# Performance work log

Hardware: AMD Instinct MI355X
Metric: run time of the kernel (lower is better)

Reference implementation:

```python
import jax, jax.numpy as jnp
import numpy as np

B, S, H, ZD, IN = 256, 64, 128, 128, 2


def _gru_cell(x, h, W_ih, W_hh, b_ih, b_hh):
    # PyTorch GRU cell math
    gi = x @ W_ih.T + b_ih
    gh = h @ W_hh.T + b_hh
    i_r, i_z, i_n = jnp.split(gi, 3, axis=-1)
    h_r, h_z, h_n = jnp.split(gh, 3, axis=-1)
    r = jax.nn.sigmoid(i_r + h_r)
    z = jax.nn.sigmoid(i_z + h_z)
    n = jnp.tanh(i_n + r * h_n)
    return (1.0 - z) * n + z * h


def setup_inputs() -> dict:
    key = jax.random.key(0)
    ks = jax.random.split(key, 20)
    instance = jax.random.uniform(ks[0], (B, S, IN), dtype=jnp.float32)
    # solution must be a valid tour (permutation per batch row)
    solution = jax.vmap(lambda k: jax.random.permutation(k, S))(
        jax.random.split(ks[1], B)).astype(jnp.int32)
    Z = jax.random.normal(ks[2], (B, ZD), dtype=jnp.float32)
    instance_hidden = jax.random.normal(ks[3], (B, S, H), dtype=jnp.float32)
    last_hh = jnp.zeros((B, H), jnp.float32)
    s = 0.1
    params = dict(
        W_emb=jax.random.normal(ks[4], (IN, H), jnp.float32) * s,
        b_emb=jnp.zeros((H,), jnp.float32),
        W_ih=jax.random.normal(ks[5], (3 * H, H), jnp.float32) * s,
        W_hh=jax.random.normal(ks[6], (3 * H, H), jnp.float32) * s,
        b_ih=jnp.zeros((3 * H,), jnp.float32),
        b_hh=jnp.zeros((3 * H,), jnp.float32),
        W_a=jax.random.normal(ks[7], (2 * H, H), jnp.float32) * s,
        v_a=jax.random.normal(ks[8], (H,), jnp.float32) * s,
        W1=jax.random.normal(ks[9], (2 * H + ZD, 2 * H), jnp.float32) * s,
        b1=jnp.zeros((2 * H,), jnp.float32),
        W2=jax.random.normal(ks[10], (2 * H, H), jnp.float32) * s,
        b2=jnp.zeros((H,), jnp.float32),
        Wp=jax.random.normal(ks[11], (2 * H, H), jnp.float32) * s,
        vp=jax.random.normal(ks[12], (H,), jnp.float32) * s,
    )
    return dict(instance=instance, solution=solution, Z=Z,
                instance_hidden=instance_hidden, last_hh=last_hh, **params)


def reference(instance, solution, Z, instance_hidden, last_hh,
              W_emb, b_emb, W_ih, W_hh, b_ih, b_hh,
              W_a, v_a, W1, b1, W2, b2, Wp, vp):
    b, s, _ = instance.shape
    barange = jnp.arange(b)
    mask0 = jnp.ones((b, s), instance.dtype).at[barange, solution[:, 0]].set(0.0)
    ref0 = instance[barange, solution[:, 0]]  # [B, IN]

    def step(carry, ptr_j):
        h, mask, ref_in = carry
        ref_h = ref_in @ W_emb + b_emb                       # [B,H] reference embedding
        h = _gru_cell(ref_h, h, W_ih, W_hh, b_ih, b_hh)      # [B,H] rnn step
        # encoder attention over static instance_hidden
        ha = jnp.concatenate([instance_hidden,
                              jnp.broadcast_to(h[:, None, :], instance_hidden.shape)], axis=2)
        attn = jax.nn.softmax(jnp.tanh(ha @ W_a) @ v_a, axis=1)      # [B,S]
        context = jnp.einsum('bs,bsh->bh', attn, instance_hidden)    # [B,H]
        fc_in = jnp.concatenate([context, Z, ref_h], axis=1)         # [B,2H+ZD]
        fco = (fc_in @ W1 + b1) @ W2 + b2                            # [B,H] fc1 -> fc2 (no activation)
        hp = jnp.concatenate([instance_hidden,
                              jnp.broadcast_to(fco[:, None, :], instance_hidden.shape)], axis=2)
        logits = jnp.tanh(hp @ Wp) @ vp                              # [B,S] pointer scores
        logprobs = jax.nn.log_softmax(logits + jnp.log(mask), axis=1)
        logp = logprobs[barange, ptr_j]                              # teacher-forced log-prob
        pred = jnp.argmax(logprobs, axis=1)
        mask = mask.at[barange, ptr_j].set(0.0)
        ref_in = instance[barange, ptr_j]
        return (h, mask, ref_in), (pred, logp)

    ptrs = solution[:, 1:].T                                         # [S-1, B]
    _, (preds, logps) = jax.lax.scan(step, (last_hh, mask0, ref0), ptrs)
    tour_idx = jnp.concatenate([solution[:, :1], preds.T.astype(solution.dtype)], axis=1)
    tour_logp = logps.T                                              # [B, S-1]
    return tour_idx, tour_logp
```

## Files before the change

### kernel.cpp

```cpp
#include <hip/hip_runtime.h>
#include <math.h>

#define NB 256
#define NS 64
#define NH 128
#define NZ 128
#define NSTEPS 63
#define HP 144
#define PP 132
#define SP 68

#define OFF_PREA 0
#define OFF_PREP 8448
#define OFF_WN   0
#define OFF_HALL 16896
#define OFF_ATTH 26112
#define OFF_SCOR 34560
#define OFF_U    38912
#define OFF_VA   39296
#define OFF_VPV  39424
#define OFF_REFX 39552
#define OFF_REFY 39616
#define OFF_SOL  39680
#define OFF_RANK 39744
#define OFF_SVA  39808
#define OFF_SVP  39809
#define SM_FLOATS 39812
#define OFF_GPRE 34560
#define OFF_BHH  35712

#define WS_WF   0
#define WS_WZ   16384
#define WS_U    32768
#define WS_GPRE 33152
#define WS_FLOATS 34304

__device__ __forceinline__ int padh(int i) { return i + ((i >> 5) << 2); }

__device__ __forceinline__ float ftanh(float x) {
  float e = __expf(2.0f * x);
  return 1.0f - 2.0f * __builtin_amdgcn_rcpf(e + 1.0f);
}
__device__ __forceinline__ float fsigm(float x) {
  return __builtin_amdgcn_rcpf(1.0f + __expf(-x));
}

#define PIN8(a, i)                                                          \
  asm volatile("" : "+v"((a)[(i)]), "+v"((a)[(i) + 1]), "+v"((a)[(i) + 2]), \
                    "+v"((a)[(i) + 3]), "+v"((a)[(i) + 4]),                 \
                    "+v"((a)[(i) + 5]), "+v"((a)[(i) + 6]),                 \
                    "+v"((a)[(i) + 7]))

__global__ __launch_bounds__(128, 1) void fold_kernel(
    const float* __restrict__ W1, const float* __restrict__ W2,
    const float* __restrict__ Wp, const float* __restrict__ W_ih,
    const float* __restrict__ W_emb, const float* __restrict__ b_emb,
    const float* __restrict__ b_ih, const float* __restrict__ b1,
    const float* __restrict__ b2, float* __restrict__ ws) {
  __shared__ float srow[NH];
  __shared__ float amS[256];
  const int g = blockIdx.x;
  const int o = threadIdx.x;
  if (g < 256) {
    const int r = (g < 128) ? g : (NH + (g - 128));
    const float* w1r = W1 + r * 256;
    float acc = 0.f;
#pragma unroll 16
    for (int m = 0; m < 256; ++m) acc += w1r[m] * W2[m * NH + o];
    srow[o] = acc;
    __syncthreads();
    float wf = 0.f;
#pragma unroll 16
    for (int j = 0; j < NH; ++j) wf += srow[j] * Wp[(NH + j) * NH + o];
    if (g < 128) ws[WS_WF + g * NH + o] = wf;
    else         ws[WS_WZ + (g - 128) * NH + o] = wf;
    if (g >= 1 && g <= 3) {
      const int row = (g - 1) * NH + o;
      const float* wi = W_ih + row * NH;
      float g0 = 0.f, g1 = 0.f, g2 = 0.f;
#pragma unroll 8
      for (int k4 = 0; k4 < 32; ++k4) {
        float4 w = *(const float4*)(wi + 4 * k4);
        float4 e0 = *(const float4*)(W_emb + 4 * k4);
        float4 e1 = *(const float4*)(W_emb + NH + 4 * k4);
        float4 eb = *(const float4*)(b_emb + 4 * k4);
        g0 += w.x * e0.x + w.y * e0.y + w.z * e0.z + w.w * e0.w;
        g1 += w.x * e1.x + w.y * e1.y + w.z * e1.z + w.w * e1.w;
        g2 += w.x * eb.x + w.y * eb.y + w.z * eb.z + w.w * eb.w;
      }
      ws[WS_GPRE + row] = g0;
      ws[WS_GPRE + 384 + row] = g1;
      ws[WS_GPRE + 768 + row] = g2 + b_ih[row];
    }
  } else {
    const int c = g - 256;
    const float* ev = (c == 0) ? W_emb : (c == 1) ? (W_emb + NH) : b_emb;
#pragma unroll
    for (int half = 0; half < 2; ++half) {
      const int m = o + 128 * half;
      float a = 0.f;
#pragma unroll 8
      for (int k = 0; k < NH; ++k) a += ev[k] * W1[(2 * NH + k) * 256 + m];
      amS[m] = (c == 2) ? (a + b1[m]) : a;
    }
    __syncthreads();
    float vv = (c == 2) ? b2[o] : 0.f;
#pragma unroll 16
    for (int m = 0; m < 256; ++m) vv += amS[m] * W2[m * NH + o];
    srow[o] = vv;
    __syncthreads();
    float U = 0.f;
#pragma unroll 16
    for (int j = 0; j < NH; ++j) U += srow[j] * Wp[(NH + j) * NH + o];
    ws[WS_U + c * NH + o] = U;
  }
}

__global__ __launch_bounds__(1024, 1) void decoder_kernel(
    const float* __restrict__ instance, const int* __restrict__ solution,
    const float* __restrict__ Z, const float* __restrict__ IH,
    const float* __restrict__ last_hh, const float* __restrict__ W_hh,
    const float* __restrict__ b_hh, const float* __restrict__ W_a,
    const float* __restrict__ v_a, const float* __restrict__ Wp,
    const float* __restrict__ vp, const float* __restrict__ ws,
    float* __restrict__ out) {
  extern __shared__ float sm[];
  int* soli = (int*)(sm + OFF_SOL);
  int* ranki = (int*)(sm + OFF_RANK);
  const int b = blockIdx.x;
  const int t = threadIdx.x;
  const float* ihb = IH + b * NS * NH;

  const int oc = t >> 3, qc = t & 7;
  const int oq = (t & 31) * 4, jg = t >> 5;
  const int jj = t >> 4, sq = t & 15;

  if (t < NS) {
    int sv = solution[b * NS + t];
    soli[t] = sv;
    ranki[sv] = t;
    sm[OFF_REFX + t] = instance[(b * NS + sv) * 2 + 0];
    sm[OFF_REFY + t] = instance[(b * NS + sv) * 2 + 1];
  }
  if (t < NH) {
    sm[OFF_VA + t] = v_a[t];
    sm[OFF_VPV + t] = vp[t];
    sm[OFF_HALL + padh(t)] = last_hh[b * NH + t];
  }
  if (t < 128) {
    const float* vsrc = (t < 64) ? v_a : vp;
    int u = t & 63;
    float s2 = vsrc[u] + vsrc[u + 64];
#pragma unroll
    for (int off = 32; off > 0; off >>= 1) s2 += __shfl_xor(s2, off);
    if (u == 0) sm[(t < 64) ? OFF_SVA : OFF_SVP] = s2;
  }
  if (t < 384) sm[OFF_BHH + t] = b_hh[t];
  for (int i = t; i < 1152; i += 1024) sm[OFF_GPRE + i] = ws[WS_GPRE + i];
  if (t < 256) sm[OFF_U + t] = ws[WS_U + t];
  {
    const float* zb = Z + b * NZ;
    float acc = 0.f;
#pragma unroll 4
    for (int u = 0; u < 16; ++u) {
      int k = 16 * qc + u;
      acc += zb[k] * ws[WS_WZ + k * NH + oc];
    }
    acc += __shfl_xor(acc, 1); acc += __shfl_xor(acc, 2); acc += __shfl_xor(acc, 4);
    if (qc == 0) sm[OFF_U + 2 * NH + oc] = ws[WS_U + 2 * NH + oc] + acc;
  }
  if (t < 512) {
    const int o4 = t >> 2, q4 = t & 3;
    const float* wnp = W_hh + (2 * NH + o4) * NH + 32 * q4;
#pragma unroll
    for (int u4 = 0; u4 < 8; ++u4) {
      float4 w = *(const float4*)(wnp + 4 * u4);
      sm[OFF_WN + t * 33 + 4 * u4 + 0] = w.x;
      sm[OFF_WN + t * 33 + 4 * u4 + 1] = w.y;
      sm[OFF_WN + t * 33 + 4 * u4 + 2] = w.z;
      sm[OFF_WN + t * 33 + 4 * u4 + 3] = w.w;
    }
  }
  if (t == 0) out[b * NS] = (float)soli[0];
  __syncthreads();

  {
    float whr[16], whz[16];
    {
      const float* br = W_hh + oc * NH + 16 * qc;
      const float* bz = W_hh + (NH + oc) * NH + 16 * qc;
#pragma unroll
      for (int u4 = 0; u4 < 4; ++u4) {
        float4 r4 = *(const float4*)(br + 4 * u4);
        float4 z4 = *(const float4*)(bz + 4 * u4);
        whr[4 * u4 + 0] = r4.x; whr[4 * u4 + 1] = r4.y;
        whr[4 * u4 + 2] = r4.z; whr[4 * u4 + 3] = r4.w;
        whz[4 * u4 + 0] = z4.x; whz[4 * u4 + 1] = z4.y;
        whz[4 * u4 + 2] = z4.z; whz[4 * u4 + 3] = z4.w;
      }
    }
    PIN8(whr, 0); PIN8(whr, 8);
    PIN8(whz, 0); PIN8(whz, 8);
    const float* wn = sm + OFF_WN + (oc * 4 + (qc >> 1)) * 33 + (qc & 1) * 16;
    const int hoffc = padh(16 * qc);
    const float bhr = sm[OFF_BHH + oc];
    const float bhz = sm[OFF_BHH + NH + oc];
    const float bhn = sm[OFF_BHH + 2 * NH + oc];
    const float gr0 = sm[OFF_GPRE + oc];
    const float gr1 = sm[OFF_GPRE + 384 + oc];
    const float gr2 = sm[OFF_GPRE + 768 + oc];
    const float gz0 = sm[OFF_GPRE + NH + oc];
    const float gz1 = sm[OFF_GPRE + 384 + NH + oc];
    const float gz2 = sm[OFF_GPRE + 768 + NH + oc];
    const float gn0 = sm[OFF_GPRE + 2 * NH + oc];
    const float gn1 = sm[OFF_GPRE + 384 + 2 * NH + oc];
    const float gn2 = sm[OFF_GPRE + 768 + 2 * NH + oc];
#pragma unroll 1
    for (int j = 1; j <= NSTEPS; ++j) {
      float ar = 0.f, az = 0.f, an = 0.f;
      const float* hp = sm + OFF_HALL + (j - 1) * HP + hoffc;
#pragma unroll
      for (int u = 0; u < 4; ++u) {
        float4 hv = *(const float4*)(hp + 4 * u);
        ar += hv.x * whr[4 * u] + hv.y * whr[4 * u + 1] +
              hv.z * whr[4 * u + 2] + hv.w * whr[4 * u + 3];
        az += hv.x * whz[4 * u] + hv.y * whz[4 * u + 1] +
              hv.z * whz[4 * u + 2] + hv.w * whz[4 * u + 3];
        an += hv.x * wn[4 * u] + hv.y * wn[4 * u + 1] +
              hv.z * wn[4 * u + 2] + hv.w * wn[4 * u + 3];
      }
      ar += __shfl_xor(ar, 1); ar += __shfl_xor(ar, 2); ar += __shfl_xor(ar, 4);
      az += __shfl_xor(az, 1); az += __shfl_xor(az, 2); az += __shfl_xor(az, 4);
      an += __shfl_xor(an, 1); an += __shfl_xor(an, 2); an += __shfl_xor(an, 4);
      if (qc == 0) {
        float r0 = sm[OFF_REFX + (j - 1)], r1 = sm[OFF_REFY + (j - 1)];
        float gir = r0 * gr0 + r1 * gr1 + gr2;
        float giz = r0 * gz0 + r1 * gz1 + gz2;
        float gin = r0 * gn0 + r1 * gn1 + gn2;
        float r = fsigm(gir + ar + bhr);
        float z = fsigm(giz + az + bhz);
        float n = ftanh(gin + r * (an + bhn));
        float hold = sm[OFF_HALL + (j - 1) * HP + padh(oc)];
        sm[OFF_HALL + j * HP + padh(oc)] = (1.f - z) * n + z * hold;
      }
      __syncthreads();
    }
  }

  for (int i = 4 * t; i < NS * NH; i += 4096)
    *(float4*)(sm + OFF_ATTH + i) = *(const float4*)(ihb + i);
  __syncthreads();
  {
    const int jx = t & 127, sg = t >> 7;
    float accA[8], accP[8];
#pragma unroll
    for (int si = 0; si < 8; ++si) { accA[si] = 0.f; accP[si] = 0.f; }
#pragma unroll 2
    for (int k4 = 0; k4 < 32; ++k4) {
      const int k = 4 * k4;
      float wa0 = W_a[(k + 0) * NH + jx];
      float wa1 = W_a[(k + 1) * NH + jx];
      float wa2 = W_a[(k + 2) * NH + jx];
      float wa3 = W_a[(k + 3) * NH + jx];
      float wp0 = Wp[(k + 0) * NH + jx];
      float wp1 = Wp[(k + 1) * NH + jx];
      float wp2 = Wp[(k + 2) * NH + jx];
      float wp3 = Wp[(k + 3) * NH + jx];
#pragma unroll
      for (int si = 0; si < 8; ++si) {
        float4 ih = *(const float4*)(sm + OFF_ATTH + (sg * 8 + si) * NH + k);
        accA[si] += ih.x * wa0 + ih.y * wa1 + ih.z * wa2 + ih.w * wa3;
        accP[si] += ih.x * wp0 + ih.y * wp1 + ih.z * wp2 + ih.w * wp3;
      }
    }
#pragma unroll
    for (int si = 0; si < 8; ++si) {
      sm[OFF_PREA + (sg * 8 + si) * PP + jx] = __expf(2.f * accA[si]);
      sm[OFF_PREP + (sg * 8 + si) * PP + jx] = __expf(2.f * accP[si]);
    }
  }
  __syncthreads();

  {
    float4 acc[2];
    acc[0] = (float4){0.f, 0.f, 0.f, 0.f};
    acc[1] = (float4){0.f, 0.f, 0.f, 0.f};
    const float* wbase = W_a + NH * NH + oq;
#pragma unroll 4
    for (int k4 = 0; k4 < 32; ++k4) {
      int k = 4 * k4;
      int hoff = k + 4 * (k4 >> 3);
      float4 w0 = *(const float4*)(wbase + (k + 0) * NH);
      float4 w1 = *(const float4*)(wbase + (k + 1) * NH);
      float4 w2 = *(const float4*)(wbase + (k + 2) * NH);
      float4 w3 = *(const float4*)(wbase + (k + 3) * NH);
#pragma unroll
      for (int i = 0; i < 2; ++i) {
        float4 hv = *(const float4*)(sm + OFF_HALL + (jg + 32 * i) * HP + hoff);
        acc[i].x += hv.x * w0.x + hv.y * w1.x + hv.z * w2.x + hv.w * w3.x;
        acc[i].y += hv.x * w0.y + hv.y * w1.y + hv.z * w2.y + hv.w * w3.y;
        acc[i].z += hv.x * w0.z + hv.y * w1.z + hv.z * w2.z + hv.w * w3.z;
        acc[i].w += hv.x * w0.w + hv.y * w1.w + hv.z * w2.w + hv.w * w3.w;
      }
    }
#pragma unroll
    for (int i = 0; i < 2; ++i) {
      float4 tv;
      tv.x = __expf(2.f * acc[i].x); tv.y = __expf(2.f * acc[i].y);
      tv.z = __expf(2.f * acc[i].z); tv.w = __expf(2.f * acc[i].w);
      *(float4*)(sm + OFF_ATTH + (jg + 32 * i) * PP + oq) = tv;
    }
  }
  __syncthreads();

  {
    const float sva = sm[OFF_SVA];
    const float* ah = sm + OFF_ATTH + jj * PP;
    float accv[4] = {0.f, 0.f, 0.f, 0.f};
#pragma unroll 2
    for (int k4 = 0; k4 < 32; ++k4) {
      float4 h = *(const float4*)(ah + 4 * k4);
      float4 v = *(const float4*)(sm + OFF_VA + 4 * k4);
#pragma unroll
      for (int i = 0; i < 4; ++i) {
        float4 a = *(const float4*)(sm + OFF_PREA + (sq + 16 * i) * PP + 4 * k4);
        accv[i] += v.x * __builtin_amdgcn_rcpf(fmaf(a.x, h.x, 1.f)) +
                   v.y * __builtin_amdgcn_rcpf(fmaf(a.y, h.y, 1.f)) +
                   v.z * __builtin_amdgcn_rcpf(fmaf(a.z, h.z, 1.f)) +
                   v.w * __builtin_amdgcn_rcpf(fmaf(a.w, h.w, 1.f));
      }
    }
#pragma unroll
    for (int i = 0; i < 4; ++i) accv[i] = sva - 2.f * accv[i];
    float m = fmaxf(fmaxf(accv[0], accv[1]), fmaxf(accv[2], accv[3]));
    m = fmaxf(m, __shfl_xor(m, 1));
    m = fmaxf(m, __shfl_xor(m, 2));
    m = fmaxf(m, __shfl_xor(m, 4));
    m = fmaxf(m, __shfl_xor(m, 8));
    float p0 = __expf(accv[0] - m), p1 = __expf(accv[1] - m);
    float p2 = __expf(accv[2] - m), p3 = __expf(accv[3] - m);
    float ssum = (p0 + p1) + (p2 + p3);
    ssum += __shfl_xor(ssum, 1); ssum += __shfl_xor(ssum, 2);
    ssum += __shfl_xor(ssum, 4); ssum += __shfl_xor(ssum, 8);
    sm[OFF_SCOR + jj * SP + sq + 0]  = p0 / ssum;
    sm[OFF_SCOR + jj * SP + sq + 16] = p1 / ssum;
    sm[OFF_SCOR + jj * SP + sq + 32] = p2 / ssum;
    sm[OFF_SCOR + jj * SP + sq + 48] = p3 / ssum;
  }
  __syncthreads();

  {
    float4 acc[2];
    acc[0] = (float4){0.f, 0.f, 0.f, 0.f};
    acc[1] = (float4){0.f, 0.f, 0.f, 0.f};
    const float* ibase = ihb + oq;
#pragma unroll 4
    for (int s4 = 0; s4 < 16; ++s4) {
      int s = 4 * s4;
      float4 x0 = *(const float4*)(ibase + (s + 0) * NH);
      float4 x1 = *(const float4*)(ibase + (s + 1) * NH);
      float4 x2 = *(const float4*)(ibase + (s + 2) * NH);
      float4 x3 = *(const float4*)(ibase + (s + 3) * NH);
#pragma unroll
      for (int i = 0; i < 2; ++i) {
        const float* at = sm + OFF_SCOR + (jg + 32 * i) * SP + s;
        float a0 = at[0], a1 = at[1], a2 = at[2], a3 = at[3];
        acc[i].x += a0 * x0.x + a1 * x1.x + a2 * x2.x + a3 * x3.x;
        acc[i].y += a0 * x0.y + a1 * x1.y + a2 * x2.y + a3 * x3.y;
        acc[i].z += a0 * x0.z + a1 * x1.z + a2 * x2.z + a3 * x3.z;
        acc[i].w += a0 * x0.w + a1 * x1.w + a2 * x2.w + a3 * x3.w;
      }
    }
#pragma unroll
    for (int i = 0; i < 2; ++i)
      *(float4*)(sm + OFF_PREA + (jg + 32 * i) * PP + oq) = acc[i];
  }
  __syncthreads();

  {
    float4 acc[2];
    acc[0] = (float4){0.f, 0.f, 0.f, 0.f};
    acc[1] = (float4){0.f, 0.f, 0.f, 0.f};
    const float* wfb = ws + WS_WF + oq;
#pragma unroll 4
    for (int k4 = 0; k4 < 32; ++k4) {
      int k = 4 * k4;
      float4 w0 = *(const float4*)(wfb + (k + 0) * NH);
      float4 w1 = *(const float4*)(wfb + (k + 1) * NH);
      float4 w2 = *(const float4*)(wfb + (k + 2) * NH);
      float4 w3 = *(const float4*)(wfb + (k + 3) * NH);
#pragma unroll
      for (int i = 0; i < 2; ++i) {
        float4 cv = *(const float4*)(sm + OFF_PREA + (jg + 32 * i) * PP + k);
        acc[i].x += cv.x * w0.x + cv.y * w1.x + cv.z * w2.x + cv.w * w3.x;
        acc[i].y += cv.x * w0.y + cv.y * w1.y + cv.z * w2.y + cv.w * w3.y;
        acc[i].z += cv.x * w0.z + cv.y * w1.z + cv.z * w2.z + cv.w * w3.z;
        acc[i].w += cv.x * w0.w + cv.y * w1.w + cv.z * w2.w + cv.w * w3.w;
      }
    }
    float4 u0 = *(const float4*)(sm + OFF_U + oq);
    float4 u1 = *(const float4*)(sm + OFF_U + NH + oq);
    float4 u2 = *(const float4*)(sm + OFF_U + 2 * NH + oq);
#pragma unroll
    for (int i = 0; i < 2; ++i) {
      int j = jg + 32 * i;
      int jm = (j > 0) ? (j - 1) : 0;
      float rx = sm[OFF_REFX + jm], ry = sm[OFF_REFY + jm];
      float4 r;
      r.x = __expf(2.f * (acc[i].x + rx * u0.x + ry * u1.x + u2.x));
      r.y = __expf(2.f * (acc[i].y + rx * u0.y + ry * u1.y + u2.y));
      r.z = __expf(2.f * (acc[i].z + rx * u0.z + ry * u1.z + u2.z));
      r.w = __expf(2.f * (acc[i].w + rx * u0.w + ry * u1.w + u2.w));
      *(float4*)(sm + OFF_ATTH + j * PP + oq) = r;
    }
  }
  __syncthreads();

  {
    const float svp = sm[OFF_SVP];
    const float* ph = sm + OFF_ATTH + jj * PP;
    float accv[4] = {0.f, 0.f, 0.f, 0.f};
#pragma unroll 2
    for (int k4 = 0; k4 < 32; ++k4) {
      float4 h = *(const float4*)(ph + 4 * k4);
      float4 v = *(const float4*)(sm + OFF_VPV + 4 * k4);
#pragma unroll
      for (int i = 0; i < 4; ++i) {
        float4 a = *(const float4*)(sm + OFF_PREP + (sq + 16 * i) * PP + 4 * k4);
        accv[i] += v.x * __builtin_amdgcn_rcpf(fmaf(a.x, h.x, 1.f)) +
                   v.y * __builtin_amdgcn_rcpf(fmaf(a.y, h.y, 1.f)) +
                   v.z * __builtin_amdgcn_rcpf(fmaf(a.z, h.z, 1.f)) +
                   v.w * __builtin_amdgcn_rcpf(fmaf(a.w, h.w, 1.f));
      }
    }
#pragma unroll
    for (int i = 0; i < 4; ++i)
      sm[OFF_SCOR + jj * SP + sq + 16 * i] = svp - 2.f * accv[i];
  }
  __syncthreads();

  {
    float ml[4];
    float m = -INFINITY;
    int mi = 127;
#pragma unroll
    for (int i = 0; i < 4; ++i) {
      int s = sq + 16 * i;
      float lg = sm[OFF_SCOR + jj * SP + s];
      ml[i] = (ranki[s] >= jj) ? lg : -INFINITY;
      if (ml[i] > m) { m = ml[i]; mi = s; }
    }
#pragma unroll
    for (int off = 1; off <= 8; off <<= 1) {
      float om = __shfl_xor(m, off);
      int oi = __shfl_xor(mi, off);
      if (om > m || (om == m && oi < mi)) { m = om; mi = oi; }
    }
    float ssum = 0.f;
#pragma unroll
    for (int i = 0; i < 4; ++i) ssum += __expf(ml[i] - m);
    ssum += __shfl_xor(ssum, 1); ssum += __shfl_xor(ssum, 2);
    ssum += __shfl_xor(ssum, 4); ssum += __shfl_xor(ssum, 8);
    if (sq == 0 && jj >= 1) {
      out[b * NS + jj] = (float)mi;
      float pv = sm[OFF_SCOR + jj * SP + soli[jj]];
      out[NB * NS + b * NSTEPS + (jj - 1)] = pv - m - __logf(ssum);
    }
  }
}

extern "C" void kernel_launch(void* const* d_in, const int* in_sizes, int n_in,
                              void* d_out, int out_size, void* d_ws,
                              size_t ws_size, hipStream_t stream) {
  (void)in_sizes; (void)n_in; (void)out_size; (void)ws_size;
  const float* instance = (const float*)d_in[0];
  const int*   solution = (const int*)d_in[1];
  const float* Z        = (const float*)d_in[2];
  const float* IH       = (const float*)d_in[3];
  const float* last_hh  = (const float*)d_in[4];
  const float* W_emb    = (const float*)d_in[5];
  const float* b_emb    = (const float*)d_in[6];
  const float* W_ih     = (const float*)d_in[7];
  const float* W_hh     = (const float*)d_in[8];
  const float* b_ih     = (const float*)d_in[9];
  const float* b_hh     = (const float*)d_in[10];
  const float* W_a      = (const float*)d_in[11];
  const float* v_a      = (const float*)d_in[12];
  const float* W1       = (const float*)d_in[13];
  const float* b1       = (const float*)d_in[14];
  const float* W2       = (const float*)d_in[15];
  const float* b2       = (const float*)d_in[16];
  const float* Wp       = (const float*)d_in[17];
  const float* vp       = (const float*)d_in[18];
  float* out = (float*)d_out;
  float* ws = (float*)d_ws;

  fold_kernel<<<259, 128, 0, stream>>>(W1, W2, Wp, W_ih, W_emb, b_emb, b_ih,
                                       b1, b2, ws);

  const int shmem = SM_FLOATS * 4;
  static_assert(SM_FLOATS * 4 <= 160 * 1024, "LDS overlay too big");
  hipFuncSetAttribute((const void*)decoder_kernel,
                      hipFuncAttributeMaxDynamicSharedMemorySize, shmem);
  decoder_kernel<<<NB, 1024, shmem, stream>>>(
      instance, solution, Z, IH, last_hh, W_hh, b_hh, W_a, v_a, Wp, vp, ws,
      out);
}
```

Measured before the change: 290.4 us.

## Fuse weight-folding prologue into decoder kernel via cooperative grid sync

Removes the separate fold kernel launch and computes the folded weight products inside the decoder kernel. Each of the 256 blocks handles one folded row, using 1024 threads and split-k reductions through shared memory. A cooperative grid-wide sync then publishes the results before decoding starts. This saves a kernel launch and the gap between kernels, at the cost of a cooperative launch, a grid barrier, and a requirement that all 256 blocks be co-resident.

```diff
diff --git a/kernel.cpp b/kernel.cpp
--- a/kernel.cpp
+++ b/kernel.cpp
@@ -1,5 +1,8 @@
 #include <hip/hip_runtime.h>
+#include <hip/hip_cooperative_groups.h>
 #include <math.h>
+
+namespace cg = cooperative_groups;
 
 #define NB 256
 #define NS 64
@@ -51,78 +54,17 @@
                     "+v"((a)[(i) + 5]), "+v"((a)[(i) + 6]),                 \
                     "+v"((a)[(i) + 7]))
 
-__global__ __launch_bounds__(128, 1) void fold_kernel(
-    const float* __restrict__ W1, const float* __restrict__ W2,
-    const float* __restrict__ Wp, const float* __restrict__ W_ih,
-    const float* __restrict__ W_emb, const float* __restrict__ b_emb,
-    const float* __restrict__ b_ih, const float* __restrict__ b1,
-    const float* __restrict__ b2, float* __restrict__ ws) {
-  __shared__ float srow[NH];
-  __shared__ float amS[256];
-  const int g = blockIdx.x;
-  const int o = threadIdx.x;
-  if (g < 256) {
-    const int r = (g < 128) ? g : (NH + (g - 128));
-    const float* w1r = W1 + r * 256;
-    float acc = 0.f;
-#pragma unroll 16
-    for (int m = 0; m < 256; ++m) acc += w1r[m] * W2[m * NH + o];
-    srow[o] = acc;
-    __syncthreads();
-    float wf = 0.f;
-#pragma unroll 16
-    for (int j = 0; j < NH; ++j) wf += srow[j] * Wp[(NH + j) * NH + o];
-    if (g < 128) ws[WS_WF + g * NH + o] = wf;
-    else         ws[WS_WZ + (g - 128) * NH + o] = wf;
-    if (g >= 1 && g <= 3) {
-      const int row = (g - 1) * NH + o;
-      const float* wi = W_ih + row * NH;
-      float g0 = 0.f, g1 = 0.f, g2 = 0.f;
-#pragma unroll 8
-      for (int k4 = 0; k4 < 32; ++k4) {
-        float4 w = *(const float4*)(wi + 4 * k4);
-        float4 e0 = *(const float4*)(W_emb + 4 * k4);
-        float4 e1 = *(const float4*)(W_emb + NH + 4 * k4);
-        float4 eb = *(const float4*)(b_emb + 4 * k4);
-        g0 += w.x * e0.x + w.y * e0.y + w.z * e0.z + w.w * e0.w;
-        g1 += w.x * e1.x + w.y * e1.y + w.z * e1.z + w.w * e1.w;
-        g2 += w.x * eb.x + w.y * eb.y + w.z * eb.z + w.w * eb.w;
-      }
-      ws[WS_GPRE + row] = g0;
-      ws[WS_GPRE + 384 + row] = g1;
-      ws[WS_GPRE + 768 + row] = g2 + b_ih[row];
-    }
-  } else {
-    const int c = g - 256;
-    const float* ev = (c == 0) ? W_emb : (c == 1) ? (W_emb + NH) : b_emb;
-#pragma unroll
-    for (int half = 0; half < 2; ++half) {
-      const int m = o + 128 * half;
-      float a = 0.f;
-#pragma unroll 8
-      for (int k = 0; k < NH; ++k) a += ev[k] * W1[(2 * NH + k) * 256 + m];
-      amS[m] = (c == 2) ? (a + b1[m]) : a;
-    }
-    __syncthreads();
-    float vv = (c == 2) ? b2[o] : 0.f;
-#pragma unroll 16
-    for (int m = 0; m < 256; ++m) vv += amS[m] * W2[m * NH + o];
-    srow[o] = vv;
-    __syncthreads();
-    float U = 0.f;
-#pragma unroll 16
-    for (int j = 0; j < NH; ++j) U += srow[j] * Wp[(NH + j) * NH + o];
-    ws[WS_U + c * NH + o] = U;
-  }
-}
-
 __global__ __launch_bounds__(1024, 1) void decoder_kernel(
     const float* __restrict__ instance, const int* __restrict__ solution,
     const float* __restrict__ Z, const float* __restrict__ IH,
-    const float* __restrict__ last_hh, const float* __restrict__ W_hh,
+    const float* __restrict__ last_hh, const float* __restrict__ W_emb,
+    const float* __restrict__ b_emb, const float* __restrict__ W_ih,
+    const float* __restrict__ W_hh, const float* __restrict__ b_ih,
     const float* __restrict__ b_hh, const float* __restrict__ W_a,
-    const float* __restrict__ v_a, const float* __restrict__ Wp,
-    const float* __restrict__ vp, const float* __restrict__ ws,
+    const float* __restrict__ v_a, const float* __restrict__ W1,
+    const float* __restrict__ b1, const float* __restrict__ W2,
+    const float* __restrict__ b2, const float* __restrict__ Wp,
+    const float* __restrict__ vp, float* __restrict__ ws,
     float* __restrict__ out) {
   extern __shared__ float sm[];
   int* soli = (int*)(sm + OFF_SOL);
@@ -134,6 +76,121 @@
   const int oc = t >> 3, qc = t & 7;
   const int oq = (t & 31) * 4, jg = t >> 5;
   const int jj = t >> 4, sq = t & 15;
+
+  {
+    const int o = t & 127, mg = t >> 7;
+    const int r = (b < 128) ? b : (NH + b - 128);
+    const float* w1r = W1 + r * 256;
+    float part = 0.f;
+#pragma unroll 8
+    for (int u = 0; u < 32; ++u) {
+      int m = 32 * mg + u;
+      part += w1r[m] * W2[m * NH + o];
+    }
+    sm[t] = part;
+    __syncthreads();
+    if (t < NH) {
+      float s1 = 0.f;
+#pragma unroll
+      for (int g2 = 0; g2 < 8; ++g2) s1 += sm[g2 * 128 + t];
+      sm[1024 + t] = s1;
+    }
+    __syncthreads();
+    float p2 = 0.f;
+#pragma unroll 4
+    for (int u = 0; u < 16; ++u) {
+      int j = 16 * mg + u;
+      p2 += sm[1024 + j] * Wp[(NH + j) * NH + o];
+    }
+    __syncthreads();
+    sm[t] = p2;
+    __syncthreads();
+    if (t < NH) {
+      float s2 = 0.f;
+#pragma unroll
+      for (int g2 = 0; g2 < 8; ++g2) s2 += sm[g2 * 128 + t];
+      if (b < 128) ws[WS_WF + b * NH + t] = s2;
+      else         ws[WS_WZ + (b - 128) * NH + t] = s2;
+    }
+    if (b >= 1 && b <= 3) {
+      __syncthreads();
+      const float* wi = W_ih + ((b - 1) * NH + o) * NH;
+      float g0 = 0.f, g1 = 0.f, g2v = 0.f;
+#pragma unroll 4
+      for (int u = 0; u < 16; ++u) {
+        int k = 16 * mg + u;
+        float w = wi[k];
+        g0 += w * W_emb[k];
+        g1 += w * W_emb[NH + k];
+        g2v += w * b_emb[k];
+      }
+      sm[t] = g0; sm[1024 + t] = g1; sm[2048 + t] = g2v;
+      __syncthreads();
+      if (t < 384) {
+        int c = t >> 7, o2 = t & 127;
+        const float* src = sm + c * 1024;
+        float s = 0.f;
+#pragma unroll
+        for (int g2 = 0; g2 < 8; ++g2) s += src[g2 * 128 + o2];
+        int row = (b - 1) * NH + o2;
+        if (c == 2) s += b_ih[row];
+        ws[WS_GPRE + c * 384 + row] = s;
+      }
+    }
+    if (b >= 4 && b <= 6) {
+      __syncthreads();
+      const int c = b - 4;
+      const float* ev = (c == 0) ? W_emb : (c == 1) ? (W_emb + NH) : b_emb;
+      const int m = t & 255, kg = t >> 8;
+      float pa = 0.f;
+#pragma unroll 8
+      for (int u = 0; u < 32; ++u) {
+        int k = 32 * kg + u;
+        pa += ev[k] * W1[(2 * NH + k) * 256 + m];
+      }
+      sm[t] = pa;
+      __syncthreads();
+      if (t < 256) {
+        float am = sm[t] + sm[256 + t] + sm[512 + t] + sm[768 + t];
+        if (c == 2) am += b1[t];
+        sm[1024 + t] = am;
+      }
+      __syncthreads();
+      float pv = 0.f;
+#pragma unroll 8
+      for (int u = 0; u < 32; ++u) {
+        int m2 = 32 * mg + u;
+        pv += sm[1024 + m2] * W2[m2 * NH + o];
+      }
+      __syncthreads();
+      sm[t] = pv;
+      __syncthreads();
+      if (t < NH) {
+        float v = 0.f;
+#pragma unroll
+        for (int g2 = 0; g2 < 8; ++g2) v += sm[g2 * 128 + t];
+        if (c == 2) v += b2[t];
+        sm[1280 + t] = v;
+      }
+      __syncthreads();
+      float pu = 0.f;
+#pragma unroll 4
+      for (int u = 0; u < 16; ++u) {
+        int j = 16 * mg + u;
+        pu += sm[1280 + j] * Wp[(NH + j) * NH + o];
+      }
+      __syncthreads();
+      sm[t] = pu;
+      __syncthreads();
+      if (t < NH) {
+        float U = 0.f;
+#pragma unroll
+        for (int g2 = 0; g2 < 8; ++g2) U += sm[g2 * 128 + t];
+        ws[WS_U + c * NH + t] = U;
+      }
+    }
+  }
+  cg::this_grid().sync();
 
   if (t < NS) {
     int sv = solution[b * NS + t];
@@ -495,14 +552,16 @@
   float* out = (float*)d_out;
   float* ws = (float*)d_ws;
 
-  fold_kernel<<<259, 128, 0, stream>>>(W1, W2, Wp, W_ih, W_emb, b_emb, b_ih,
-                                       b1, b2, ws);
-
   const int shmem = SM_FLOATS * 4;
   static_assert(SM_FLOATS * 4 <= 160 * 1024, "LDS overlay too big");
   hipFuncSetAttribute((const void*)decoder_kernel,
                       hipFuncAttributeMaxDynamicSharedMemorySize, shmem);
-  decoder_kernel<<<NB, 1024, shmem, stream>>>(
-      instance, solution, Z, IH, last_hh, W_hh, b_hh, W_a, v_a, Wp, vp, ws,
-      out);
+  void* args[] = {(void*)&instance, (void*)&solution, (void*)&Z, (void*)&IH,
+                  (void*)&last_hh, (void*)&W_emb, (void*)&b_emb, (void*)&W_ih,
+                  (void*)&W_hh, (void*)&b_ih, (void*)&b_hh, (void*)&W_a,
+                  (void*)&v_a, (void*)&W1, (void*)&b1, (void*)&W2,
+                  (void*)&b2, (void*)&Wp, (void*)&vp, (void*)&ws,
+                  (void*)&out};
+  hipLaunchCooperativeKernel((const void*)decoder_kernel, dim3(NB), dim3(1024),
+                             args, shmem, stream);
 }
```

Result: slower. 333.0 us (+14.6%).
